# Optimization experiments

Measured on AMD Instinct MI355X. Metric: run time of the kernel, lower is better.

The kernel has to match this reference:

```python
import jax, jax.numpy as jnp
import numpy as np

H = 128  # h_size


def setup_inputs() -> dict:
    key = jax.random.key(0)
    ks = jax.random.split(key, 6)
    depth, n_trees = 16, 4
    N = 2 ** depth - 1          # nodes per complete binary tree
    T = n_trees * N             # total nodes
    return {
        "iou": jax.random.normal(ks[0], (T, 3 * H), dtype=jnp.float32),
        "h": jax.random.normal(ks[1], (T, H), dtype=jnp.float32),
        "c": jax.random.normal(ks[2], (T, H), dtype=jnp.float32),
        "W_iou": jax.random.normal(ks[3], (3 * H, 2 * H), dtype=jnp.float32) * 0.05,
        "b_iou": jnp.zeros((3 * H,), dtype=jnp.float32),
        "W_f": jax.random.normal(ks[4], (2 * H, 2 * H), dtype=jnp.float32) * 0.05,
        "b_f": jnp.zeros((2 * H,), dtype=jnp.float32),
        "depth": depth,
        "n_trees": n_trees,
    }


def _gates(iou, b_iou):
    i, o, u = jnp.split(iou + b_iou, 3, axis=1)
    return jax.nn.sigmoid(i), jax.nn.sigmoid(o), jnp.tanh(u)


def reference(iou, h, c, W_iou, b_iou, W_f, b_f, depth, n_trees):
    N = 2 ** depth - 1
    offs = (jnp.arange(n_trees) * N)[:, None]  # per-tree node offsets

    # --- leaf frontier: no messages -> apply_node_func only (keeps initial iou, c) ---
    l = depth - 1
    idx = (offs + jnp.arange(2 ** l - 1, 2 ** (l + 1) - 1)[None, :]).reshape(-1)
    i, o, u = _gates(iou[idx], b_iou)
    c_new = i * u + c[idx]
    h = h.at[idx].set(o * jnp.tanh(c_new))
    c = c.at[idx].set(c_new)

    # --- internal levels, bottom-up (level-parallel topological propagation) ---
    for l in range(depth - 2, -1, -1):
        loc = jnp.arange(2 ** l - 1, 2 ** (l + 1) - 1)
        idx = (offs + loc[None, :]).reshape(-1)
        lidx = (offs + (2 * loc + 1)[None, :]).reshape(-1)  # left child
        ridx = lidx + 1                                      # right child
        # reduce_func: gather children, forget gates, sum-reduce c, new iou
        h_cat = jnp.concatenate([h[lidx], h[ridx]], axis=-1)          # [n, 2H]
        f = jax.nn.sigmoid(h_cat @ W_f.T + b_f).reshape(-1, 2, H)     # [n, 2, H]
        c_kids = jnp.stack([c[lidx], c[ridx]], axis=1)                # [n, 2, H]
        c_red = jnp.sum(f * c_kids, axis=1)                           # [n, H]
        iou_red = h_cat @ W_iou.T                                     # [n, 3H]
        # apply_node_func
        i, o, u = _gates(iou_red, b_iou)
        c_new = i * u + c_red
        h = h.at[idx].set(o * jnp.tanh(c_new))
        c = c.at[idx].set(c_new)
    return h
```

## Files before the change

### kernel.cpp

```cpp
#include <hip/hip_runtime.h>

#define HH   128
#define H2   256
#define H3   384
#define NPT  65535
#define TPB  512

typedef __bf16    bf16x8 __attribute__((ext_vector_type(8)));
typedef float     f32x4  __attribute__((ext_vector_type(4)));
typedef _Float16  f16x4  __attribute__((ext_vector_type(4)));
typedef _Float16  half_t;

__device__ unsigned short Wb_g[640 * 256];

__device__ __forceinline__ float fsig(float x)  { return 1.0f / (1.0f + __expf(-x)); }
__device__ __forceinline__ float ftanh(float x) { return 1.0f - 2.0f / (__expf(2.0f * x) + 1.0f); }
__device__ __forceinline__ unsigned short f2bf(float f) {
    unsigned u = __float_as_uint(f);
    u += 0x7fffu + ((u >> 16) & 1u);
    return (unsigned short)(u >> 16);
}
__device__ __forceinline__ int swz(int off) { return off ^ (((off >> 9) & 7) << 4); }

__global__ __launch_bounds__(256) void conv_k(const float* __restrict__ W_iou,
                                              const float* __restrict__ W_f)
{
    int t    = blockIdx.x * 256 + threadIdx.x;
    int base = t * 4;
    int j = base >> 8, k = base & 255;
    const float* src = (j < H3) ? (W_iou + j * H2 + k)
                                : (W_f + (j - H3) * H2 + k);
    float4 v = *(const float4*)src;
    ushort4 p;
    p.x = f2bf(v.x); p.y = f2bf(v.y); p.z = f2bf(v.z); p.w = f2bf(v.w);
    *(ushort4*)(Wb_g + base) = p;
}

#define GATES5(PI, PO, PU, PL, PR, CL, CR, HV, CV) \
    { CV = fsig(PI) * ftanh(PU) + fsig(PL) * (CL) + fsig(PR) * (CR); \
      HV = fsig(PO) * ftanh(CV); }

__global__ __launch_bounds__(TPB, 4) void leaf14_k(
    const float* __restrict__ iou, const float* __restrict__ c_in,
    const float* __restrict__ b_iou, const float* __restrict__ b_f,
    float* __restrict__ h_g, half_t* __restrict__ c_ws,
    unsigned short* __restrict__ h_bf)
{
    __shared__ __align__(16) unsigned short A_lds[32 * H2];
    __shared__ __align__(16) half_t         C_lds[64 * HH];

    const int tid = threadIdx.x;
    const int w  = tid >> 6;
    const int lr = tid & 15;
    const int lc = (tid & 63) >> 4;
    const int ee = w * 16 + lr;
    const int node0 = blockIdx.x * 32;
    const int tree  = node0 >> 14;
    const int lbase = tree * NPT + 32767 + 2 * (node0 & 16383);

#pragma unroll
    for (int it = 0; it < 4; ++it) {
        int p   = tid + TPB * it;
        int row = p >> 5;
        int e4  = p & 31;
        int grow = lbase + row;
        const float* ip = iou + (size_t)grow * H3 + e4 * 4;
        float4 vi = *(const float4*)(ip);
        float4 vo = *(const float4*)(ip + HH);
        float4 vu = *(const float4*)(ip + 2 * HH);
        float4 vc = *(const float4*)(c_in + (size_t)grow * HH + e4 * 4);
        float4 bi = *(const float4*)(b_iou + e4 * 4);
        float4 bo = *(const float4*)(b_iou + HH + e4 * 4);
        float4 bu = *(const float4*)(b_iou + 2 * HH + e4 * 4);

        float4 hn, cn;
#define DOL(X) { float iv = fsig(vi.X + bi.X); float ov = fsig(vo.X + bo.X); \
                 float uv = ftanh(vu.X + bu.X); float cv = iv * uv + vc.X;   \
                 cn.X = cv; hn.X = ov * ftanh(cv); }
        DOL(x) DOL(y) DOL(z) DOL(w)
#undef DOL
        *(float4*)(h_g + (size_t)grow * HH + e4 * 4) = hn;
        f16x4 cf; cf.x = (half_t)cn.x; cf.y = (half_t)cn.y;
        cf.z = (half_t)cn.z; cf.w = (half_t)cn.w;
        *(f16x4*)(C_lds + row * HH + e4 * 4) = cf;
        int m = row >> 1, half = row & 1;
        uint2 pk;
        pk.x = (unsigned)f2bf(hn.x) | ((unsigned)f2bf(hn.y) << 16);
        pk.y = (unsigned)f2bf(hn.z) | ((unsigned)f2bf(hn.w) << 16);
        int byte = (m * 512 + half * 256 + e4 * 8) ^ ((m & 7) << 4);
        *(uint2*)((char*)A_lds + byte) = pk;
    }
    __syncthreads();

    f32x4 acc[2][5] = {};
    const unsigned short* Wp = Wb_g + ee * H2 + lc * 8;
#pragma unroll
    for (int kk = 0; kk < 8; ++kk) {
        bf16x8 a0 = *(const bf16x8*)((const char*)A_lds + swz(lr * 512 + kk * 64 + lc * 16));
        bf16x8 a1 = *(const bf16x8*)((const char*)A_lds + swz((16 + lr) * 512 + kk * 64 + lc * 16));
#pragma unroll
        for (int g = 0; g < 5; ++g) {
            bf16x8 b = *(const bf16x8*)(Wp + g * HH * H2 + kk * 32);
            acc[0][g] = __builtin_amdgcn_mfma_f32_16x16x32_bf16(a0, b, acc[0][g], 0, 0, 0);
            acc[1][g] = __builtin_amdgcn_mfma_f32_16x16x32_bf16(a1, b, acc[1][g], 0, 0, 0);
        }
    }

    const float bi = b_iou[ee], bo = b_iou[HH + ee], bu = b_iou[2 * HH + ee];
    const float bl = b_f[ee],   br = b_f[HH + ee];
#pragma unroll
    for (int mt = 0; mt < 2; ++mt)
#pragma unroll
        for (int r = 0; r < 4; ++r) {
            int q    = mt * 16 + lc * 4 + r;
            int node = node0 + q;
            int base = tree * NPT + 16383 + (node & 16383);
            int o    = base * HH + ee;
            float cl = (float)C_lds[(2 * q) * HH + ee];
            float cr = (float)C_lds[(2 * q + 1) * HH + ee];
            float hv, cv;
            GATES5(acc[mt][0][r] + bi, acc[mt][1][r] + bo, acc[mt][2][r] + bu,
                   acc[mt][3][r] + bl, acc[mt][4][r] + br, cl, cr, hv, cv);
            h_g[o]  = hv;
            c_ws[o] = (half_t)cv;
            h_bf[o] = f2bf(hv);
        }
}

__global__ __launch_bounds__(TPB, 4) void level_k(
    int lvl,
    const float* __restrict__ b_iou, const float* __restrict__ b_f,
    float* __restrict__ h_g, half_t* __restrict__ c_ws,
    unsigned short* __restrict__ h_bf)
{
    __shared__ __align__(16) unsigned short A_lds[32 * H2];

    const int tid = threadIdx.x;
    const int w  = tid >> 6;
    const int lr = tid & 15;
    const int lc = (tid & 63) >> 4;
    const int ee = w * 16 + lr;
    const int node0 = blockIdx.x * 32;
    const int loc0  = (1 << lvl) - 1;
    const int lmask = loc0;

#pragma unroll
    for (int it = 0; it < 2; ++it) {
        int item = tid + TPB * it;
        int m = item >> 5, u = item & 31;
        int node = node0 + m;
        int tree = node >> lvl;
        int loc  = loc0 + (node & lmask);
        int coff = (tree * NPT + 2 * loc + 1 + (u >> 4)) * HH + (u & 15) * 8;
        uint4 v = *(const uint4*)(h_bf + coff);
        *(uint4*)((char*)A_lds + swz(m * 512 + u * 16)) = v;
    }
    __syncthreads();

    int   rofs[2][4];
    float clv[2][4], crv[2][4];
#pragma unroll
    for (int mt = 0; mt < 2; ++mt)
#pragma unroll
        for (int r = 0; r < 4; ++r) {
            int node = node0 + mt * 16 + lc * 4 + r;
            int tree = node >> lvl;
            int loc  = loc0 + (node & lmask);
            int base = tree * NPT + loc;
            int lrow = base + loc + 1;
            rofs[mt][r] = base * HH + ee;
            clv[mt][r] = (float)c_ws[lrow * HH + ee];
            crv[mt][r] = (float)c_ws[lrow * HH + HH + ee];
        }

    f32x4 acc[2][5] = {};
    const unsigned short* Wp = Wb_g + ee * H2 + lc * 8;
#pragma unroll
    for (int kk = 0; kk < 8; ++kk) {
        bf16x8 a0 = *(const bf16x8*)((const char*)A_lds + swz(lr * 512 + kk * 64 + lc * 16));
        bf16x8 a1 = *(const bf16x8*)((const char*)A_lds + swz((16 + lr) * 512 + kk * 64 + lc * 16));
#pragma unroll
        for (int g = 0; g < 5; ++g) {
            bf16x8 b = *(const bf16x8*)(Wp + g * HH * H2 + kk * 32);
            acc[0][g] = __builtin_amdgcn_mfma_f32_16x16x32_bf16(a0, b, acc[0][g], 0, 0, 0);
            acc[1][g] = __builtin_amdgcn_mfma_f32_16x16x32_bf16(a1, b, acc[1][g], 0, 0, 0);
        }
    }

    const float bi = b_iou[ee], bo = b_iou[HH + ee], bu = b_iou[2 * HH + ee];
    const float bl = b_f[ee],   br = b_f[HH + ee];
#pragma unroll
    for (int mt = 0; mt < 2; ++mt)
#pragma unroll
        for (int r = 0; r < 4; ++r) {
            float hv, cv;
            GATES5(acc[mt][0][r] + bi, acc[mt][1][r] + bo, acc[mt][2][r] + bu,
                   acc[mt][3][r] + bl, acc[mt][4][r] + br, clv[mt][r], crv[mt][r], hv, cv);
            int o = rofs[mt][r];
            h_g[o]  = hv;
            c_ws[o] = (half_t)cv;
            h_bf[o] = f2bf(hv);
        }
}

__global__ __launch_bounds__(TPB, 2) void solo_k(
    const float* __restrict__ b_iou, const float* __restrict__ b_f,
    float* __restrict__ h_g, half_t* __restrict__ c_ws,
    const unsigned short* __restrict__ h_bf)
{
    __shared__ __align__(16) unsigned char hb[32768];

    const int tid = threadIdx.x;
    const int w = tid >> 6, lr = tid & 15, lc = (tid & 63) >> 4;
    const int ee = w * 16 + lr;
    const int tb = blockIdx.x * NPT;
    const float bi = b_iou[ee], bo = b_iou[HH + ee], bu = b_iou[2 * HH + ee];
    const float bl = b_f[ee],   br = b_f[HH + ee];

    bf16x8 Bf[5][8];
    const unsigned short* Wp = Wb_g + ee * H2 + lc * 8;
#pragma unroll
    for (int g = 0; g < 5; ++g)
#pragma unroll
        for (int kk = 0; kk < 8; ++kk)
            Bf[g][kk] = *(const bf16x8*)(Wp + g * HH * H2 + kk * 32);

#pragma unroll
    for (int it = 0; it < 2; ++it) {
        int p = tid + TPB * it;
        int cc = p >> 4, q = p & 15;
        uint4 v = *(const uint4*)(h_bf + (tb + 63 + cc) * HH + q * 8);
        *(uint4*)(hb + swz(p * 16)) = v;
    }

#pragma unroll 1
    for (int l = 5; l >= 0; --l) {
        const int nl     = 1 << l;
        const int loc0   = nl - 1;
        const int cloc0  = 2 * nl - 1;
        const int cbase  = (l & 1) ? 0 : 16384;
        const int obase  = cbase ^ 16384;
        const bool mt1   = (nl > 16);

        __syncthreads();

        f32x4 acc[2][5] = {};
#pragma unroll
        for (int kk = 0; kk < 8; ++kk) {
            bf16x8 a0 = *(const bf16x8*)(hb + cbase + swz(lr * 512 + kk * 64 + lc * 16));
#pragma unroll
            for (int g = 0; g < 5; ++g)
                acc[0][g] = __builtin_amdgcn_mfma_f32_16x16x32_bf16(a0, Bf[g][kk], acc[0][g], 0, 0, 0);
            if (mt1) {
                bf16x8 a1 = *(const bf16x8*)(hb + cbase + swz((16 + lr) * 512 + kk * 64 + lc * 16));
#pragma unroll
                for (int g = 0; g < 5; ++g)
                    acc[1][g] = __builtin_amdgcn_mfma_f32_16x16x32_bf16(a1, Bf[g][kk], acc[1][g], 0, 0, 0);
            }
        }
        __syncthreads();

#pragma unroll
        for (int mt = 0; mt < 2; ++mt)
#pragma unroll
            for (int r = 0; r < 4; ++r) {
                int j = mt * 16 + lc * 4 + r;
                if (j >= nl) continue;
                int row  = tb + loc0 + j;
                int lrow = tb + cloc0 + 2 * j;
                float cl = (float)c_ws[lrow * HH + ee];
                float cr = (float)c_ws[lrow * HH + HH + ee];
                float hv, cv;
                GATES5(acc[mt][0][r] + bi, acc[mt][1][r] + bo, acc[mt][2][r] + bu,
                       acc[mt][3][r] + bl, acc[mt][4][r] + br, cl, cr, hv, cv);
                h_g[row * HH + ee]  = hv;
                c_ws[row * HH + ee] = (half_t)cv;
                *(unsigned short*)(hb + obase + swz(j * 256 + ee * 2)) = f2bf(hv);
            }
    }
}

extern "C" void kernel_launch(void* const* d_in, const int* in_sizes, int n_in,
                              void* d_out, int out_size, void* d_ws, size_t ws_size,
                              hipStream_t stream)
{
    const float* iou   = (const float*)d_in[0];
    const float* c_in  = (const float*)d_in[2];
    const float* W_iou = (const float*)d_in[3];
    const float* b_iou = (const float*)d_in[4];
    const float* W_f   = (const float*)d_in[5];
    const float* b_f   = (const float*)d_in[6];
    float* h_out = (float*)d_out;
    half_t* c_ws = (half_t*)d_ws;
    unsigned short* h_bf = (unsigned short*)((char*)d_ws + (size_t)72 * 1024 * 1024);

    conv_k<<<160, 256, 0, stream>>>(W_iou, W_f);
    leaf14_k<<<2048, TPB, 0, stream>>>(iou, c_in, b_iou, b_f, h_out, c_ws, h_bf);
    for (int l = 13; l >= 6; --l) {
        int blocks = (4 << l) / 32;
        level_k<<<blocks, TPB, 0, stream>>>(l, b_iou, b_f, h_out, c_ws, h_bf);
    }
    solo_k<<<4, TPB, 0, stream>>>(b_iou, b_f, h_out, c_ws, h_bf);
}
```

Measured before the change: 346.7 us.

## Fuse level-13 computation into leaf kernel using on-chip level-14 results

The leaf kernel now keeps its 32 level-14 outputs (bf16 h and fp16 c) in LDS and immediately computes the 16 level-13 parents of those nodes with a second MFMA pass, then writes only level-13 state to the workspace. This removes one level_k launch and the global round trip of level-14 h_bf/c_ws reads. Level-14 c and h_bf are no longer stored globally, only h_g in fp32. Bias loads and the weight pointer are hoisted to the top. The extra LDS reuse needs additional barriers, and the second MFMA pass uses only half the M tile.

```diff
diff --git a/kernel.cpp b/kernel.cpp
--- a/kernel.cpp
+++ b/kernel.cpp
@@ -40,7 +40,7 @@
     { CV = fsig(PI) * ftanh(PU) + fsig(PL) * (CL) + fsig(PR) * (CR); \
       HV = fsig(PO) * ftanh(CV); }
 
-__global__ __launch_bounds__(TPB, 4) void leaf14_k(
+__global__ __launch_bounds__(TPB, 4) void leaf1413_k(
     const float* __restrict__ iou, const float* __restrict__ c_in,
     const float* __restrict__ b_iou, const float* __restrict__ b_f,
     float* __restrict__ h_g, half_t* __restrict__ c_ws,
@@ -57,6 +57,9 @@
     const int node0 = blockIdx.x * 32;
     const int tree  = node0 >> 14;
     const int lbase = tree * NPT + 32767 + 2 * (node0 & 16383);
+    const float bi = b_iou[ee], bo = b_iou[HH + ee], bu = b_iou[2 * HH + ee];
+    const float bl = b_f[ee],   br = b_f[HH + ee];
+    const unsigned short* Wp = Wb_g + ee * H2 + lc * 8;
 
 #pragma unroll
     for (int it = 0; it < 4; ++it) {
@@ -69,13 +72,13 @@
         float4 vo = *(const float4*)(ip + HH);
         float4 vu = *(const float4*)(ip + 2 * HH);
         float4 vc = *(const float4*)(c_in + (size_t)grow * HH + e4 * 4);
-        float4 bi = *(const float4*)(b_iou + e4 * 4);
-        float4 bo = *(const float4*)(b_iou + HH + e4 * 4);
-        float4 bu = *(const float4*)(b_iou + 2 * HH + e4 * 4);
+        float4 bi4 = *(const float4*)(b_iou + e4 * 4);
+        float4 bo4 = *(const float4*)(b_iou + HH + e4 * 4);
+        float4 bu4 = *(const float4*)(b_iou + 2 * HH + e4 * 4);
 
         float4 hn, cn;
-#define DOL(X) { float iv = fsig(vi.X + bi.X); float ov = fsig(vo.X + bo.X); \
-                 float uv = ftanh(vu.X + bu.X); float cv = iv * uv + vc.X;   \
+#define DOL(X) { float iv = fsig(vi.X + bi4.X); float ov = fsig(vo.X + bo4.X); \
+                 float uv = ftanh(vu.X + bu4.X); float cv = iv * uv + vc.X;    \
                  cn.X = cv; hn.X = ov * ftanh(cv); }
         DOL(x) DOL(y) DOL(z) DOL(w)
 #undef DOL
@@ -93,7 +96,6 @@
     __syncthreads();
 
     f32x4 acc[2][5] = {};
-    const unsigned short* Wp = Wb_g + ee * H2 + lc * 8;
 #pragma unroll
     for (int kk = 0; kk < 8; ++kk) {
         bf16x8 a0 = *(const bf16x8*)((const char*)A_lds + swz(lr * 512 + kk * 64 + lc * 16));
@@ -105,9 +107,11 @@
             acc[1][g] = __builtin_amdgcn_mfma_f32_16x16x32_bf16(a1, b, acc[1][g], 0, 0, 0);
         }
     }
-
-    const float bi = b_iou[ee], bo = b_iou[HH + ee], bu = b_iou[2 * HH + ee];
-    const float bl = b_f[ee],   br = b_f[HH + ee];
+    __syncthreads();
+
+    unsigned char* A13 = (unsigned char*)A_lds;
+    half_t*        C13 = (half_t*)((unsigned char*)A_lds + 8192);
+
 #pragma unroll
     for (int mt = 0; mt < 2; ++mt)
 #pragma unroll
@@ -115,16 +119,45 @@
             int q    = mt * 16 + lc * 4 + r;
             int node = node0 + q;
             int base = tree * NPT + 16383 + (node & 16383);
-            int o    = base * HH + ee;
             float cl = (float)C_lds[(2 * q) * HH + ee];
             float cr = (float)C_lds[(2 * q + 1) * HH + ee];
             float hv, cv;
             GATES5(acc[mt][0][r] + bi, acc[mt][1][r] + bo, acc[mt][2][r] + bu,
                    acc[mt][3][r] + bl, acc[mt][4][r] + br, cl, cr, hv, cv);
-            h_g[o]  = hv;
-            c_ws[o] = (half_t)cv;
-            h_bf[o] = f2bf(hv);
-        }
+            h_g[base * HH + ee] = hv;
+            int j = q >> 1, half = q & 1;
+            int byte = (j * 512 + half * 256 + ee * 2) ^ ((j & 7) << 4);
+            *(unsigned short*)(A13 + byte) = f2bf(hv);
+            C13[q * HH + ee] = (half_t)cv;
+        }
+    __syncthreads();
+
+    f32x4 acc3[5] = {};
+#pragma unroll
+    for (int kk = 0; kk < 8; ++kk) {
+        bf16x8 a0 = *(const bf16x8*)(A13 + swz(lr * 512 + kk * 64 + lc * 16));
+#pragma unroll
+        for (int g = 0; g < 5; ++g) {
+            bf16x8 b = *(const bf16x8*)(Wp + g * HH * H2 + kk * 32);
+            acc3[g] = __builtin_amdgcn_mfma_f32_16x16x32_bf16(a0, b, acc3[g], 0, 0, 0);
+        }
+    }
+    const int n13_0 = blockIdx.x * 16;
+#pragma unroll
+    for (int r = 0; r < 4; ++r) {
+        int j    = lc * 4 + r;
+        int node = n13_0 + j;
+        int base = tree * NPT + 8191 + (node & 8191);
+        int o    = base * HH + ee;
+        float cl = (float)C13[(2 * j) * HH + ee];
+        float cr = (float)C13[(2 * j + 1) * HH + ee];
+        float hv, cv;
+        GATES5(acc3[0][r] + bi, acc3[1][r] + bo, acc3[2][r] + bu,
+               acc3[3][r] + bl, acc3[4][r] + br, cl, cr, hv, cv);
+        h_g[o]  = hv;
+        c_ws[o] = (half_t)cv;
+        h_bf[o] = f2bf(hv);
+    }
 }
 
 __global__ __launch_bounds__(TPB, 4) void level_k(
@@ -295,8 +328,8 @@
     unsigned short* h_bf = (unsigned short*)((char*)d_ws + (size_t)72 * 1024 * 1024);
 
     conv_k<<<160, 256, 0, stream>>>(W_iou, W_f);
-    leaf14_k<<<2048, TPB, 0, stream>>>(iou, c_in, b_iou, b_f, h_out, c_ws, h_bf);
-    for (int l = 13; l >= 6; --l) {
+    leaf1413_k<<<2048, TPB, 0, stream>>>(iou, c_in, b_iou, b_f, h_out, c_ws, h_bf);
+    for (int l = 12; l >= 6; --l) {
         int blocks = (4 << l) / 32;
         level_k<<<blocks, TPB, 0, stream>>>(l, b_iou, b_f, h_out, c_ws, h_bf);
     }
```

After: 368.2 us. +6.2%, slower.

## Shrink leaf kernel tiles to 16 nodes per 256-thread block, add nontemporal streaming

Applied to the files above, without the earlier changes.

The fused leaf-plus-level-14 kernel now handles 16 parent nodes per 256-thread block instead of 32 nodes per 512 threads, so twice as many smaller blocks are launched. Each wave now covers two 16-column groups of output features with one shared A fragment rather than two node tiles sharing one B fragment, which changes the reuse pattern in the MFMA loop. The streaming iou/c loads and leaf h stores switch to nontemporal builtins to reduce cache pollution. The finer grid should improve occupancy and load balance, at the cost of doubling weight-fragment loads per node.

```diff
diff --git a/kernel.cpp b/kernel.cpp
--- a/kernel.cpp
+++ b/kernel.cpp
@@ -40,46 +40,45 @@
     { CV = fsig(PI) * ftanh(PU) + fsig(PL) * (CL) + fsig(PR) * (CR); \
       HV = fsig(PO) * ftanh(CV); }
 
-__global__ __launch_bounds__(TPB, 4) void leaf14_k(
+__global__ __launch_bounds__(256, 4) void leaf14_k(
     const float* __restrict__ iou, const float* __restrict__ c_in,
     const float* __restrict__ b_iou, const float* __restrict__ b_f,
     float* __restrict__ h_g, half_t* __restrict__ c_ws,
     unsigned short* __restrict__ h_bf)
 {
-    __shared__ __align__(16) unsigned short A_lds[32 * H2];
-    __shared__ __align__(16) half_t         C_lds[64 * HH];
+    __shared__ __align__(16) unsigned short A_lds[16 * H2];
+    __shared__ __align__(16) half_t         C_lds[32 * HH];
 
     const int tid = threadIdx.x;
     const int w  = tid >> 6;
     const int lr = tid & 15;
     const int lc = (tid & 63) >> 4;
-    const int ee = w * 16 + lr;
-    const int node0 = blockIdx.x * 32;
+    const int node0 = blockIdx.x * 16;
     const int tree  = node0 >> 14;
     const int lbase = tree * NPT + 32767 + 2 * (node0 & 16383);
 
 #pragma unroll
     for (int it = 0; it < 4; ++it) {
-        int p   = tid + TPB * it;
+        int p   = tid + 256 * it;
         int row = p >> 5;
         int e4  = p & 31;
         int grow = lbase + row;
         const float* ip = iou + (size_t)grow * H3 + e4 * 4;
-        float4 vi = *(const float4*)(ip);
-        float4 vo = *(const float4*)(ip + HH);
-        float4 vu = *(const float4*)(ip + 2 * HH);
-        float4 vc = *(const float4*)(c_in + (size_t)grow * HH + e4 * 4);
-        float4 bi = *(const float4*)(b_iou + e4 * 4);
-        float4 bo = *(const float4*)(b_iou + HH + e4 * 4);
-        float4 bu = *(const float4*)(b_iou + 2 * HH + e4 * 4);
-
-        float4 hn, cn;
-#define DOL(X) { float iv = fsig(vi.X + bi.X); float ov = fsig(vo.X + bo.X); \
-                 float uv = ftanh(vu.X + bu.X); float cv = iv * uv + vc.X;   \
+        f32x4 vi = __builtin_nontemporal_load((const f32x4*)(ip));
+        f32x4 vo = __builtin_nontemporal_load((const f32x4*)(ip + HH));
+        f32x4 vu = __builtin_nontemporal_load((const f32x4*)(ip + 2 * HH));
+        f32x4 vc = __builtin_nontemporal_load((const f32x4*)(c_in + (size_t)grow * HH + e4 * 4));
+        float4 bi4 = *(const float4*)(b_iou + e4 * 4);
+        float4 bo4 = *(const float4*)(b_iou + HH + e4 * 4);
+        float4 bu4 = *(const float4*)(b_iou + 2 * HH + e4 * 4);
+
+        f32x4 hn, cn;
+#define DOL(X) { float iv = fsig(vi.X + bi4.X); float ov = fsig(vo.X + bo4.X); \
+                 float uv = ftanh(vu.X + bu4.X); float cv = iv * uv + vc.X;    \
                  cn.X = cv; hn.X = ov * ftanh(cv); }
         DOL(x) DOL(y) DOL(z) DOL(w)
 #undef DOL
-        *(float4*)(h_g + (size_t)grow * HH + e4 * 4) = hn;
+        __builtin_nontemporal_store(hn, (f32x4*)(h_g + (size_t)grow * HH + e4 * 4));
         f16x4 cf; cf.x = (half_t)cn.x; cf.y = (half_t)cn.y;
         cf.z = (half_t)cn.z; cf.w = (half_t)cn.w;
         *(f16x4*)(C_lds + row * HH + e4 * 4) = cf;
@@ -93,38 +92,41 @@
     __syncthreads();
 
     f32x4 acc[2][5] = {};
-    const unsigned short* Wp = Wb_g + ee * H2 + lc * 8;
+    const unsigned short* Wp0 = Wb_g + (w * 16 + lr) * H2 + lc * 8;
+    const unsigned short* Wp1 = Wp0 + 64 * H2;
 #pragma unroll
     for (int kk = 0; kk < 8; ++kk) {
         bf16x8 a0 = *(const bf16x8*)((const char*)A_lds + swz(lr * 512 + kk * 64 + lc * 16));
-        bf16x8 a1 = *(const bf16x8*)((const char*)A_lds + swz((16 + lr) * 512 + kk * 64 + lc * 16));
 #pragma unroll
         for (int g = 0; g < 5; ++g) {
-            bf16x8 b = *(const bf16x8*)(Wp + g * HH * H2 + kk * 32);
-            acc[0][g] = __builtin_amdgcn_mfma_f32_16x16x32_bf16(a0, b, acc[0][g], 0, 0, 0);
-            acc[1][g] = __builtin_amdgcn_mfma_f32_16x16x32_bf16(a1, b, acc[1][g], 0, 0, 0);
-        }
-    }
-
-    const float bi = b_iou[ee], bo = b_iou[HH + ee], bu = b_iou[2 * HH + ee];
-    const float bl = b_f[ee],   br = b_f[HH + ee];
-#pragma unroll
-    for (int mt = 0; mt < 2; ++mt)
+            bf16x8 b0 = *(const bf16x8*)(Wp0 + g * HH * H2 + kk * 32);
+            bf16x8 b1 = *(const bf16x8*)(Wp1 + g * HH * H2 + kk * 32);
+            acc[0][g] = __builtin_amdgcn_mfma_f32_16x16x32_bf16(a0, b0, acc[0][g], 0, 0, 0);
+            acc[1][g] = __builtin_amdgcn_mfma_f32_16x16x32_bf16(a0, b1, acc[1][g], 0, 0, 0);
+        }
+    }
+
+#pragma unroll
+    for (int cg = 0; cg < 2; ++cg) {
+        const int ee = cg * 64 + w * 16 + lr;
+        const float bi = b_iou[ee], bo = b_iou[HH + ee], bu = b_iou[2 * HH + ee];
+        const float bl = b_f[ee],   br = b_f[HH + ee];
 #pragma unroll
         for (int r = 0; r < 4; ++r) {
-            int q    = mt * 16 + lc * 4 + r;
+            int q    = lc * 4 + r;
             int node = node0 + q;
             int base = tree * NPT + 16383 + (node & 16383);
             int o    = base * HH + ee;
             float cl = (float)C_lds[(2 * q) * HH + ee];
             float cr = (float)C_lds[(2 * q + 1) * HH + ee];
             float hv, cv;
-            GATES5(acc[mt][0][r] + bi, acc[mt][1][r] + bo, acc[mt][2][r] + bu,
-                   acc[mt][3][r] + bl, acc[mt][4][r] + br, cl, cr, hv, cv);
+            GATES5(acc[cg][0][r] + bi, acc[cg][1][r] + bo, acc[cg][2][r] + bu,
+                   acc[cg][3][r] + bl, acc[cg][4][r] + br, cl, cr, hv, cv);
             h_g[o]  = hv;
             c_ws[o] = (half_t)cv;
             h_bf[o] = f2bf(hv);
         }
+    }
 }
 
 __global__ __launch_bounds__(TPB, 4) void level_k(
@@ -295,7 +297,7 @@
     unsigned short* h_bf = (unsigned short*)((char*)d_ws + (size_t)72 * 1024 * 1024);
 
     conv_k<<<160, 256, 0, stream>>>(W_iou, W_f);
-    leaf14_k<<<2048, TPB, 0, stream>>>(iou, c_in, b_iou, b_f, h_out, c_ws, h_bf);
+    leaf14_k<<<4096, 256, 0, stream>>>(iou, c_in, b_iou, b_f, h_out, c_ws, h_bf);
     for (int l = 13; l >= 6; --l) {
         int blocks = (4 << l) / 32;
         level_k<<<blocks, TPB, 0, stream>>>(l, b_iou, b_f, h_out, c_ws, h_bf);
```

After: 392.5 us. 1.13x slower.
